# Optimization experiments

Measured on AMD Instinct MI355X. Metric: run time of the kernel, lower is better.

Reference implementation:

```python
import jax, jax.numpy as jnp
import numpy as np

TAU = 0.5

def setup_inputs() -> dict:
    key = jax.random.key(0)
    ks = jax.random.split(key, 20)
    B, D1, D2, E1, E2, U = 4096, 2000, 2000, 256, 256, 512
    M = E1 + E2
    s = lambda k, shp, scale=0.05: jax.random.normal(k, shp, dtype=jnp.float32) * scale
    return {
        "inputs": jax.random.normal(ks[0], (B, D1 + D2), dtype=jnp.float32),
        "h_tm1": jax.random.normal(ks[1], (B, U), dtype=jnp.float32),
        "crohis_tm": jax.random.normal(ks[2], (B, M), dtype=jnp.float32),
        "embed_weight_1": s(ks[3], (D1, E1)),
        "embed_weight_2": s(ks[4], (D2, E2)),
        "ca_1to2_w": s(ks[5], (E1, E1)),
        "ca_1to2_u": s(ks[6], (E2, E1)),
        "ca_1to2_v": s(ks[7], (E2, E1)),
        "ca_2to1_w": s(ks[8], (E2, E2)),
        "ca_2to1_u": s(ks[9], (E1, E2)),
        "ca_2to1_v": s(ks[10], (E1, E2)),
        "crohis_weight_w": s(ks[11], (M, U)),
        "crohis_bias": jnp.zeros((U,), jnp.float32),
        "crohis_decomp_weight": s(ks[12], (M, M)),
        "crohis_decomp_bias": jnp.zeros((M,), jnp.float32),
        "kernel": s(ks[13], (M, 3 * U)),
        "recurrent_kernel": s(ks[14], (U, 3 * U)),
        "bias": jnp.zeros((3 * U,), jnp.float32),
    }


def reference(inputs, h_tm1, crohis_tm,
              embed_weight_1, embed_weight_2,
              ca_1to2_w, ca_1to2_u, ca_1to2_v,
              ca_2to1_w, ca_2to1_u, ca_2to1_v,
              crohis_weight_w, crohis_bias,
              crohis_decomp_weight, crohis_decomp_bias,
              kernel, recurrent_kernel, bias):
    D1 = embed_weight_1.shape[0]
    U = recurrent_kernel.shape[0]
    # dual embedding lookups (dense multi-hot x embedding matrix)
    seqx1 = inputs[:, :D1]
    seqx2 = inputs[:, D1:]
    emb1 = seqx1 @ embed_weight_1   # [B, E1]
    emb2 = seqx2 @ embed_weight_2   # [B, E2]
    # cross-attention gates (softmax over feature axis, as K.softmax default)
    att12 = jax.nn.softmax(jnp.tanh(emb1 @ ca_1to2_w + emb2 @ ca_1to2_u) * (emb2 @ ca_1to2_v), axis=-1)
    att21 = jax.nn.softmax(jnp.tanh(emb2 @ ca_2to1_w + emb1 @ ca_2to1_u) * (emb1 @ ca_2to1_v), axis=-1)
    x = jnp.concatenate([emb1 * att12, emb2 * att21], axis=-1)  # [B, M]
    # cross-history decomposition modulating previous hidden state
    cro = jnp.tanh(crohis_tm @ crohis_decomp_weight + crohis_decomp_bias)
    h_prev = h_tm1 + jnp.tanh(cro @ crohis_weight_w + crohis_bias)
    # GRU (implementation=2, reset_after=False)
    mx = x @ kernel + bias                         # [B, 3U]
    x_z, x_r, x_h = mx[:, :U], mx[:, U:2 * U], mx[:, 2 * U:]
    mi = h_prev @ recurrent_kernel[:, :2 * U]      # [B, 2U]
    z = jax.nn.sigmoid(x_z + mi[:, :U])
    r = jax.nn.sigmoid(x_r + mi[:, U:])
    hh = jnp.tanh(x_h + (r * h_prev) @ recurrent_kernel[:, 2 * U:])
    h = z * h_prev + (1.0 - z) * hh
    # updated cross-history state (exponential moving average with tau)
    crohis_new = TAU * crohis_tm + (1.0 - TAU) * x
    return h, crohis_new
```

## Files before the change

kernel.cpp:

```cpp
#include <hip/hip_runtime.h>
#include <hip/hip_bf16.h>
#include <math.h>


#define TAU_F 0.5f

typedef __bf16 bf16x8 __attribute__((ext_vector_type(8)));
typedef __bf16 bf16x4 __attribute__((ext_vector_type(4)));
typedef float f32x4 __attribute__((ext_vector_type(4)));

__device__ __forceinline__ void gload16(const void* g, void* l) {
    __builtin_amdgcn_global_load_lds(
        (const __attribute__((address_space(1))) void*)g,
        (__attribute__((address_space(3))) void*)l, 16, 0, 0);
}

struct SubGemm {
    const void* A;
    int lda;
    int Kvalid;
    const __bf16* BT;
    int ldbt;
    float* C;
    int ldc;
    long long strideC;
    int Ksub;
    int nbx;
    int pairSplit;
    int pairAOff;
    int obf16;
};

template <bool AFP32>
__global__ __launch_bounds__(256) void gemm_dual(SubGemm g1, SubGemm g2, int blocks1)
{
    __shared__ __attribute__((aligned(16))) char lds[AFP32 ? 16384 : 12288];

    const int tid = threadIdx.x, w = tid >> 6, l = tid & 63;

    const int gx = gridDim.x;
    const int nwg = gx * (int)gridDim.y;
    const int hw = (int)blockIdx.y * gx + (int)blockIdx.x;
    const int lg = (hw & 7) * (nwg >> 3) + (hw >> 3);
    const int bxl_lin = lg % gx;
    const int by = lg / gx;

    const bool second = bxl_lin >= blocks1;
    const SubGemm& g = second ? g2 : g1;
    const int bxl = second ? bxl_lin - blocks1 : bxl_lin;
    const int ct = bxl % g.nbx, spl = bxl / g.nbx;
    const int brow = by * 64, bcol = ct * 128;
    const int k_begin = spl * g.Ksub;
    const int nt = g.Ksub >> 5;
    const int aoff = (ct >= g.pairSplit) ? g.pairAOff : 0;

    const int sbr = w * 32 + (l >> 2);
    const int seg = (l & 3) * 8;

    const __bf16* Bg0 = g.BT + (size_t)(bcol + sbr) * g.ldbt + seg + k_begin;
    const __bf16* Bg1 = Bg0 + (size_t)16 * g.ldbt;

    f32x4 acc[2][4] = {};
    const int fr = l & 15, fk = (l >> 4) * 8;
    const int wr = (w >> 1) * 32, wc = (w & 1) * 64;

    if constexpr (AFP32) {
        auto As32 = (float (*)[32])lds;
        auto Bs   = (__bf16 (*)[32])(lds + 8192);

        const float* Ar0 = (const float*)g.A + aoff
                         + (size_t)(brow + w * 16 + (l >> 3)) * g.lda;
        const float* Ar8 = Ar0 + (size_t)8 * g.lda;
        const int colLane = (l & 7) * 4;
        const int kcl4 = g.Kvalid - 4;

        for (int t = 0; t < nt; ++t) {
            const int k = t * 32;
            __syncthreads();
            int c0 = k_begin + k + colLane;
            c0 = c0 < kcl4 ? c0 : kcl4;
            gload16(Ar0 + c0, &As32[w * 16][0]);
            gload16(Ar8 + c0, &As32[w * 16 + 8][0]);
            gload16(Bg0 + k,  &Bs[w * 32][0]);
            gload16(Bg1 + k,  &Bs[w * 32 + 16][0]);
            __syncthreads();

            bf16x8 a[2], b[4];
#pragma unroll
            for (int m = 0; m < 2; ++m) {
                f32x4 lo = *(const f32x4*)&As32[wr + m * 16 + fr][fk];
                f32x4 hi = *(const f32x4*)&As32[wr + m * 16 + fr][fk + 4];
#pragma unroll
                for (int z = 0; z < 4; ++z) { a[m][z] = (__bf16)lo[z]; a[m][4 + z] = (__bf16)hi[z]; }
            }
#pragma unroll
            for (int n = 0; n < 4; ++n) b[n] = *(const bf16x8*)&Bs[wc + n * 16 + fr][fk];
#pragma unroll
            for (int m = 0; m < 2; ++m)
#pragma unroll
                for (int n = 0; n < 4; ++n)
                    acc[m][n] = __builtin_amdgcn_mfma_f32_16x16x32_bf16(a[m], b[n], acc[m][n], 0, 0, 0);
        }
    } else {
        auto As = (__bf16 (*)[32])lds;
        auto Bs = (__bf16 (*)[32])(lds + 4096);

        const int sar = w * 16 + (l >> 2);
        const __bf16* Ar = (const __bf16*)g.A + aoff
                         + (size_t)(brow + sar) * g.lda + seg + k_begin;

        for (int t = 0; t < nt; ++t) {
            const int k = t * 32;
            __syncthreads();
            gload16(Ar + k,  &As[w * 16][0]);
            gload16(Bg0 + k, &Bs[w * 32][0]);
            gload16(Bg1 + k, &Bs[w * 32 + 16][0]);
            __syncthreads();

            bf16x8 a[2], b[4];
#pragma unroll
            for (int m = 0; m < 2; ++m) a[m] = *(const bf16x8*)&As[wr + m * 16 + fr][fk];
#pragma unroll
            for (int n = 0; n < 4; ++n) b[n] = *(const bf16x8*)&Bs[wc + n * 16 + fr][fk];
#pragma unroll
            for (int m = 0; m < 2; ++m)
#pragma unroll
                for (int n = 0; n < 4; ++n)
                    acc[m][n] = __builtin_amdgcn_mfma_f32_16x16x32_bf16(a[m], b[n], acc[m][n], 0, 0, 0);
        }
    }

    const int fq = (l >> 4) * 4;
    if (g.obf16) {
        __bf16* Cb = (__bf16*)g.C + (size_t)spl * g.strideC;
#pragma unroll
        for (int m = 0; m < 2; ++m)
#pragma unroll
            for (int n = 0; n < 4; ++n)
#pragma unroll
                for (int r = 0; r < 4; ++r) {
                    int row = brow + wr + m * 16 + fq + r;
                    int col = bcol + wc + n * 16 + fr;
                    Cb[(size_t)row * g.ldc + col] = (__bf16)acc[m][n][r];
                }
    } else {
        float* C = g.C + (size_t)spl * g.strideC;
#pragma unroll
        for (int m = 0; m < 2; ++m)
#pragma unroll
            for (int n = 0; n < 4; ++n)
#pragma unroll
                for (int r = 0; r < 4; ++r) {
                    int row = brow + wr + m * 16 + fq + r;
                    int col = bcol + wc + n * 16 + fr;
                    C[(size_t)row * g.ldc + col] = acc[m][n][r];
                }
    }
}

__global__ __launch_bounds__(256) void prep_wT(
    const float* __restrict__ ew1, const float* __restrict__ ew2,
    const float* __restrict__ w12, const float* __restrict__ u12,
    const float* __restrict__ v12, const float* __restrict__ w21,
    const float* __restrict__ u21, const float* __restrict__ v21,
    const float* __restrict__ cd_w, const float* __restrict__ cw_w,
    const float* __restrict__ kern, const float* __restrict__ rkern,
    __bf16* __restrict__ WT, __bf16* __restrict__ WcatT,
    __bf16* __restrict__ cdT, __bf16* __restrict__ cwT,
    __bf16* __restrict__ kernT, __bf16* __restrict__ rkernT)
{
    __shared__ float tile[64][65];
    const int b = blockIdx.x, tid = threadIdx.x;
    const int tr = tid >> 6, tc = tid & 63;

    const float* src = nullptr;
    int ldsrc = 0, srow0 = 0, scol0 = 0, kvalid = 1 << 30;
    __bf16* dst; int ldd, n0, k0;
    bool zero = false;

    if (b < 256) {
        int q = b; n0 = (q >> 5) * 64; k0 = (q & 31) * 64;
        dst = WT; ldd = 2048; kvalid = 2000; ldsrc = 256; srow0 = k0;
        if (n0 < 256) { src = ew1; scol0 = n0; } else { src = ew2; scol0 = n0 - 256; }
    } else if (b < 384) {
        int q = b - 256; n0 = (q >> 3) * 64; k0 = (q & 7) * 64;
        dst = WcatT; ldd = 512; ldsrc = 256; srow0 = k0 & 255; scol0 = n0 & 255;
        int qn = n0 >> 8; bool khi = k0 >= 256;
        if (qn == 0)      src = khi ? u12 : w12;
        else if (qn == 1) src = khi ? w21 : u21;
        else if (qn == 2) { if (khi) src = v12; else zero = true; }
        else              { if (khi) zero = true; else src = v21; }
    } else if (b < 448) {
        int q = b - 384; n0 = (q >> 3) * 64; k0 = (q & 7) * 64;
        src = cd_w; ldsrc = 512; srow0 = k0; scol0 = n0; dst = cdT; ldd = 512;
    } else if (b < 512) {
        int q = b - 448; n0 = (q >> 3) * 64; k0 = (q & 7) * 64;
        src = cw_w; ldsrc = 512; srow0 = k0; scol0 = n0; dst = cwT; ldd = 512;
    } else if (b < 704) {
        int q = b - 512; n0 = (q >> 3) * 64; k0 = (q & 7) * 64;
        src = kern; ldsrc = 1536; srow0 = k0; scol0 = n0; dst = kernT; ldd = 512;
    } else {
        int q = b - 704; n0 = (q >> 3) * 64; k0 = (q & 7) * 64;
        src = rkern; ldsrc = 1536; srow0 = k0; scol0 = n0; dst = rkernT; ldd = 512;
    }

#pragma unroll
    for (int p = 0; p < 16; ++p) {
        int kr = p * 4 + tr;
        float v = 0.f;
        if (!zero && (srow0 + kr) < kvalid)
            v = src[(size_t)(srow0 + kr) * ldsrc + scol0 + tc];
        tile[kr][tc] = v;
    }
    __syncthreads();
#pragma unroll
    for (int p = 0; p < 16; ++p) {
        int nr = p * 4 + tr;
        dst[(size_t)(n0 + nr) * ldd + k0 + tc] = (__bf16)tile[tc][nr];
    }
}

__global__ __launch_bounds__(256) void reduce_A(
    const float* __restrict__ P12, const float* __restrict__ P4,
    const float* __restrict__ cd_b,
    __bf16* __restrict__ E, __bf16* __restrict__ cro)
{
    const int S = 1 << 21;
    int b = blockIdx.x;
    int i = (((b & 2047) * 256) + threadIdx.x) * 4;
    if (b < 2048) {
        f32x4 p0 = *(const f32x4*)(P12 + i);
        f32x4 p1 = *(const f32x4*)(P12 + S + i);
        f32x4 p2 = *(const f32x4*)(P12 + 2 * S + i);
        f32x4 p3 = *(const f32x4*)(P12 + 3 * S + i);
        __bf16 o[4];
#pragma unroll
        for (int j = 0; j < 4; ++j) o[j] = (__bf16)((p0[j] + p1[j]) + (p2[j] + p3[j]));
        *(bf16x4*)&E[i] = *(bf16x4*)o;
    } else {
        f32x4 p0 = *(const f32x4*)(P4 + i);
        f32x4 p1 = *(const f32x4*)(P4 + S + i);
        int c = i & 511;
        __bf16 o[4];
#pragma unroll
        for (int j = 0; j < 4; ++j) o[j] = (__bf16)tanhf(p0[j] + p1[j] + cd_b[c + j]);
        *(bf16x4*)&cro[i] = *(bf16x4*)o;
    }
}

__global__ __launch_bounds__(256) void fuse1(
    const __bf16* __restrict__ T, const __bf16* __restrict__ E,
    const float* __restrict__ crohis,
    const float* __restrict__ P5a, const float* __restrict__ P5b,
    const float* __restrict__ h_tm1, const float* __restrict__ cw_b,
    __bf16* __restrict__ x, float* __restrict__ cro_out,
    float* __restrict__ hprev, __bf16* __restrict__ hprev_bf)
{
    __shared__ float s4[4];
    int b = blockIdx.x;
    int j = threadIdx.x;
    if (b < 4096) {
        const __bf16* t = T + (size_t)b * 1024;
        float s12 = tanhf((float)t[j])       * (float)t[512 + j];
        float s21 = tanhf((float)t[256 + j]) * (float)t[768 + j];
        float v = s12;
#pragma unroll
        for (int o = 32; o >= 1; o >>= 1) v = fmaxf(v, __shfl_xor(v, o, 64));
        __syncthreads(); if ((j & 63) == 0) s4[j >> 6] = v; __syncthreads();
        float m12 = fmaxf(fmaxf(s4[0], s4[1]), fmaxf(s4[2], s4[3]));
        float e12 = expf(s12 - m12);
        v = e12;
#pragma unroll
        for (int o = 32; o >= 1; o >>= 1) v += __shfl_xor(v, o, 64);
        __syncthreads(); if ((j & 63) == 0) s4[j >> 6] = v; __syncthreads();
        float sum12 = s4[0] + s4[1] + s4[2] + s4[3];
        v = s21;
#pragma unroll
        for (int o = 32; o >= 1; o >>= 1) v = fmaxf(v, __shfl_xor(v, o, 64));
        __syncthreads(); if ((j & 63) == 0) s4[j >> 6] = v; __syncthreads();
        float m21 = fmaxf(fmaxf(s4[0], s4[1]), fmaxf(s4[2], s4[3]));
        float e21 = expf(s21 - m21);
        v = e21;
#pragma unroll
        for (int o = 32; o >= 1; o >>= 1) v += __shfl_xor(v, o, 64);
        __syncthreads(); if ((j & 63) == 0) s4[j >> 6] = v; __syncthreads();
        float sum21 = s4[0] + s4[1] + s4[2] + s4[3];

        size_t b0 = (size_t)b * 512 + j, b1 = b0 + 256;
        float x1 = (float)E[b0] * (e12 / sum12);
        float x2 = (float)E[b1] * (e21 / sum21);
        x[b0] = (__bf16)x1;
        x[b1] = (__bf16)x2;
        cro_out[b0] = TAU_F * crohis[b0] + (1.f - TAU_F) * x1;
        cro_out[b1] = TAU_F * crohis[b1] + (1.f - TAU_F) * x2;
    } else {
        int i = ((b - 4096) * 256 + j) * 4;
        f32x4 p0 = *(const f32x4*)(P5a + i);
        f32x4 p1 = *(const f32x4*)(P5b + i);
        f32x4 ht = *(const f32x4*)(h_tm1 + i);
        int c = i & 511;
        f32x4 o; __bf16 ob[4];
#pragma unroll
        for (int q = 0; q < 4; ++q) {
            float hv = ht[q] + tanhf(p0[q] + p1[q] + cw_b[c + q]);
            o[q] = hv; ob[q] = (__bf16)hv;
        }
        *(f32x4*)(hprev + i) = o;
        *(bf16x4*)&hprev_bf[i] = *(bf16x4*)ob;
    }
}

__global__ __launch_bounds__(256) void gates_k(
    const float* __restrict__ mx, const float* __restrict__ mi2,
    const float* __restrict__ hprev, const float* __restrict__ bias,
    __bf16* __restrict__ rh)
{
    int i = (blockIdx.x * 256 + threadIdx.x) * 4;
    int row = i >> 9, c = i & 511;
    f32x4 a  = *(const f32x4*)(mx + (size_t)row * 1536 + 512 + c);
    f32x4 m  = *(const f32x4*)(mi2 + (size_t)row * 1024 + 512 + c);
    f32x4 hp = *(const f32x4*)(hprev + i);
    f32x4 bb = *(const f32x4*)(bias + 512 + c);
    __bf16 o[4];
#pragma unroll
    for (int q = 0; q < 4; ++q) {
        float r = 1.f / (1.f + expf(-(a[q] + bb[q] + m[q])));
        o[q] = (__bf16)(r * hp[q]);
    }
    *(bf16x4*)&rh[i] = *(bf16x4*)o;
}

__global__ __launch_bounds__(256) void final_k(
    const float* __restrict__ mx, const float* __restrict__ mi2,
    const float* __restrict__ P8a, const float* __restrict__ P8b,
    const float* __restrict__ hprev, const float* __restrict__ bias,
    float* __restrict__ h)
{
    int i = (blockIdx.x * 256 + threadIdx.x) * 4;
    int row = i >> 9, c = i & 511;
    f32x4 xz = *(const f32x4*)(mx + (size_t)row * 1536 + c);
    f32x4 xh = *(const f32x4*)(mx + (size_t)row * 1536 + 1024 + c);
    f32x4 mz = *(const f32x4*)(mi2 + (size_t)row * 1024 + c);
    f32x4 p0 = *(const f32x4*)(P8a + i);
    f32x4 p1 = *(const f32x4*)(P8b + i);
    f32x4 hp = *(const f32x4*)(hprev + i);
    f32x4 bz = *(const f32x4*)(bias + c);
    f32x4 bh = *(const f32x4*)(bias + 1024 + c);
    f32x4 o;
#pragma unroll
    for (int q = 0; q < 4; ++q) {
        float z = 1.f / (1.f + expf(-(xz[q] + bz[q] + mz[q])));
        float hh = tanhf(xh[q] + bh[q] + p0[q] + p1[q]);
        o[q] = z * hp[q] + (1.f - z) * hh;
    }
    *(f32x4*)(h + i) = o;
}

extern "C" void kernel_launch(void* const* d_in, const int* in_sizes, int n_in,
                              void* d_out, int out_size, void* d_ws, size_t ws_size,
                              hipStream_t stream)
{
    (void)in_sizes; (void)n_in; (void)out_size; (void)ws_size;

    const float* inputs = (const float*)d_in[0];
    const float* h_tm1  = (const float*)d_in[1];
    const float* crohis = (const float*)d_in[2];
    const float* ew1    = (const float*)d_in[3];
    const float* ew2    = (const float*)d_in[4];
    const float* ca12w  = (const float*)d_in[5];
    const float* ca12u  = (const float*)d_in[6];
    const float* ca12v  = (const float*)d_in[7];
    const float* ca21w  = (const float*)d_in[8];
    const float* ca21u  = (const float*)d_in[9];
    const float* ca21v  = (const float*)d_in[10];
    const float* cw_w   = (const float*)d_in[11];
    const float* cw_b   = (const float*)d_in[12];
    const float* cd_w   = (const float*)d_in[13];
    const float* cd_b   = (const float*)d_in[14];
    const float* kern   = (const float*)d_in[15];
    const float* rkern  = (const float*)d_in[16];
    const float* bias   = (const float*)d_in[17];

    char* ws = (char*)d_ws;
    const size_t MB = 1 << 20;
    float*  P12      = (float*)(ws + 0);
    float*  P5       = (float*)(ws + 0);
    float*  mi2      = (float*)(ws + 0);
    __bf16* x        = (__bf16*)(ws + 16 * MB);
    __bf16* rh       = (__bf16*)(ws + 16 * MB);
    float*  hprev    = (float*)(ws + 20 * MB);
    __bf16* hprev_bf = (__bf16*)(ws + 28 * MB);
    float*  P4       = (float*)(ws + 32 * MB);
    float*  mx       = (float*)(ws + 32 * MB);
    __bf16* E        = (__bf16*)(ws + 48 * MB);
    __bf16* cro_bf   = (__bf16*)(ws + 52 * MB);
    __bf16* T        = (__bf16*)(ws + 56 * MB);
    float*  P8       = (float*)(ws + 56 * MB);
    __bf16* WT       = (__bf16*)(ws + 72 * MB);
    __bf16* WcatT    = (__bf16*)(ws + 74 * MB);
    __bf16* cdT      = (__bf16*)(ws + 75 * MB);
    __bf16* cwT      = (__bf16*)(ws + 75 * MB + 512 * 1024);
    __bf16* kernT    = (__bf16*)(ws + 76 * MB);
    __bf16* rkernT   = (__bf16*)(ws + 77 * MB + 512 * 1024);

    float* h_out   = (float*)d_out;
    float* cro_out = (float*)d_out + 2 * 1048576;

    const int BIG = 1 << 30;
    const long long S2 = 1ll << 21;

    prep_wT<<<896, 256, 0, stream>>>(ew1, ew2, ca12w, ca12u, ca12v, ca21w,
                                     ca21u, ca21v, cd_w, cw_w, kern, rkern,
                                     WT, WcatT, cdT, cwT, kernT, rkernT);

    SubGemm gA1 = { inputs, 4000, 2000, WT,  2048, P12, 512, S2, 512, 4, 2, 2000, 0 };
    SubGemm gA2 = { crohis,  512,  512, cdT,  512, P4,  512, S2, 256, 4, BIG, 0, 0 };
    gemm_dual<true><<<dim3(24, 64), 256, 0, stream>>>(gA1, gA2, 16);

    reduce_A<<<4096, 256, 0, stream>>>(P12, P4, cd_b, E, cro_bf);

    SubGemm gB1 = { E,      512, 512, WcatT, 512, (float*)T, 1024, 0,  512, 8, BIG, 0, 1 };
    SubGemm gB2 = { cro_bf, 512, 512, cwT,   512, P5,        512,  S2, 256, 4, BIG, 0, 0 };
    gemm_dual<false><<<dim3(16, 64), 256, 0, stream>>>(gB1, gB2, 8);

    fuse1<<<6144, 256, 0, stream>>>(T, E, crohis, P5, P5 + S2, h_tm1, cw_b,
                                    x, cro_out, hprev, hprev_bf);

    SubGemm gC1 = { x,        512, 512, kernT,  512, mx,  1536, 0, 512, 12, BIG, 0, 0 };
    SubGemm gC2 = { hprev_bf, 512, 512, rkernT, 512, mi2, 1024, 0, 512, 8,  BIG, 0, 0 };
    gemm_dual<false><<<dim3(20, 64), 256, 0, stream>>>(gC1, gC2, 12);

    gates_k<<<2048, 256, 0, stream>>>(mx, mi2, hprev, bias, rh);

    SubGemm gG = { rh, 512, 512, rkernT + (size_t)1024 * 512, 512, P8, 512, S2, 256, 4, BIG, 0, 0 };
    gemm_dual<false><<<dim3(8, 64), 256, 0, stream>>>(gG, gG, 8);

    final_k<<<2048, 256, 0, stream>>>(mx, mi2, P8, P8 + S2, hprev, bias, h_out);
}
```

Baseline: 143.3 us.

## Load GEMM fragments straight from global to registers and cut split-K factors

```diff
diff --git a/kernel.cpp b/kernel.cpp
--- a/kernel.cpp
+++ b/kernel.cpp
@@ -8,12 +8,6 @@
 typedef __bf16 bf16x8 __attribute__((ext_vector_type(8)));
 typedef __bf16 bf16x4 __attribute__((ext_vector_type(4)));
 typedef float f32x4 __attribute__((ext_vector_type(4)));
-
-__device__ __forceinline__ void gload16(const void* g, void* l) {
-    __builtin_amdgcn_global_load_lds(
-        (const __attribute__((address_space(1))) void*)g,
-        (__attribute__((address_space(3))) void*)l, 16, 0, 0);
-}
 
 struct SubGemm {
     const void* A;
@@ -34,8 +28,6 @@
 template <bool AFP32>
 __global__ __launch_bounds__(256) void gemm_dual(SubGemm g1, SubGemm g2, int blocks1)
 {
-    __shared__ __attribute__((aligned(16))) char lds[AFP32 ? 16384 : 12288];
-
     const int tid = threadIdx.x, w = tid >> 6, l = tid & 63;
 
     const int gx = gridDim.x;
@@ -54,80 +46,69 @@
     const int nt = g.Ksub >> 5;
     const int aoff = (ct >= g.pairSplit) ? g.pairAOff : 0;
 
-    const int sbr = w * 32 + (l >> 2);
-    const int seg = (l & 3) * 8;
-
-    const __bf16* Bg0 = g.BT + (size_t)(bcol + sbr) * g.ldbt + seg + k_begin;
-    const __bf16* Bg1 = Bg0 + (size_t)16 * g.ldbt;
-
-    f32x4 acc[2][4] = {};
     const int fr = l & 15, fk = (l >> 4) * 8;
     const int wr = (w >> 1) * 32, wc = (w & 1) * 64;
 
-    if constexpr (AFP32) {
-        auto As32 = (float (*)[32])lds;
-        auto Bs   = (__bf16 (*)[32])(lds + 8192);
-
-        const float* Ar0 = (const float*)g.A + aoff
-                         + (size_t)(brow + w * 16 + (l >> 3)) * g.lda;
-        const float* Ar8 = Ar0 + (size_t)8 * g.lda;
-        const int colLane = (l & 7) * 4;
-        const int kcl4 = g.Kvalid - 4;
-
-        for (int t = 0; t < nt; ++t) {
-            const int k = t * 32;
-            __syncthreads();
-            int c0 = k_begin + k + colLane;
-            c0 = c0 < kcl4 ? c0 : kcl4;
-            gload16(Ar0 + c0, &As32[w * 16][0]);
-            gload16(Ar8 + c0, &As32[w * 16 + 8][0]);
-            gload16(Bg0 + k,  &Bs[w * 32][0]);
-            gload16(Bg1 + k,  &Bs[w * 32 + 16][0]);
-            __syncthreads();
-
-            bf16x8 a[2], b[4];
-#pragma unroll
-            for (int m = 0; m < 2; ++m) {
-                f32x4 lo = *(const f32x4*)&As32[wr + m * 16 + fr][fk];
-                f32x4 hi = *(const f32x4*)&As32[wr + m * 16 + fr][fk + 4];
-#pragma unroll
-                for (int z = 0; z < 4; ++z) { a[m][z] = (__bf16)lo[z]; a[m][4 + z] = (__bf16)hi[z]; }
-            }
-#pragma unroll
-            for (int n = 0; n < 4; ++n) b[n] = *(const bf16x8*)&Bs[wc + n * 16 + fr][fk];
-#pragma unroll
-            for (int m = 0; m < 2; ++m)
-#pragma unroll
-                for (int n = 0; n < 4; ++n)
-                    acc[m][n] = __builtin_amdgcn_mfma_f32_16x16x32_bf16(a[m], b[n], acc[m][n], 0, 0, 0);
+    const __bf16* b0 = g.BT + (size_t)(bcol + wc +  0 + fr) * g.ldbt + k_begin + fk;
+    const __bf16* b1 = g.BT + (size_t)(bcol + wc + 16 + fr) * g.ldbt + k_begin + fk;
+    const __bf16* b2 = g.BT + (size_t)(bcol + wc + 32 + fr) * g.ldbt + k_begin + fk;
+    const __bf16* b3 = g.BT + (size_t)(bcol + wc + 48 + fr) * g.ldbt + k_begin + fk;
+
+    const __bf16* a0b = (const __bf16*)g.A + aoff + (size_t)(brow + wr +  0 + fr) * g.lda + k_begin + fk;
+    const __bf16* a1b = (const __bf16*)g.A + aoff + (size_t)(brow + wr + 16 + fr) * g.lda + k_begin + fk;
+    const float*  a0f = (const float*)g.A + aoff + (size_t)(brow + wr +  0 + fr) * g.lda;
+    const float*  a1f = (const float*)g.A + aoff + (size_t)(brow + wr + 16 + fr) * g.lda;
+    const int kcl = g.Kvalid - 8;
+
+    struct FR { bf16x8 a0, a1, b0, b1, b2, b3; };
+
+    auto ldA32 = [&](const float* rowp, int k) -> bf16x8 {
+        int c = k_begin + k + fk;
+        c = c < kcl ? c : kcl;
+        f32x4 lo = *(const f32x4*)(rowp + c);
+        f32x4 hi = *(const f32x4*)(rowp + c + 4);
+        bf16x8 r;
+#pragma unroll
+        for (int z = 0; z < 4; ++z) { r[z] = (__bf16)lo[z]; r[4 + z] = (__bf16)hi[z]; }
+        return r;
+    };
+
+    auto LD = [&](int k) -> FR {
+        FR f;
+        if constexpr (AFP32) {
+            f.a0 = ldA32(a0f, k);
+            f.a1 = ldA32(a1f, k);
+        } else {
+            f.a0 = *(const bf16x8*)(a0b + k);
+            f.a1 = *(const bf16x8*)(a1b + k);
         }
-    } else {
-        auto As = (__bf16 (*)[32])lds;
-        auto Bs = (__bf16 (*)[32])(lds + 4096);
-
-        const int sar = w * 16 + (l >> 2);
-        const __bf16* Ar = (const __bf16*)g.A + aoff
-                         + (size_t)(brow + sar) * g.lda + seg + k_begin;
-
-        for (int t = 0; t < nt; ++t) {
-            const int k = t * 32;
-            __syncthreads();
-            gload16(Ar + k,  &As[w * 16][0]);
-            gload16(Bg0 + k, &Bs[w * 32][0]);
-            gload16(Bg1 + k, &Bs[w * 32 + 16][0]);
-            __syncthreads();
-
-            bf16x8 a[2], b[4];
-#pragma unroll
-            for (int m = 0; m < 2; ++m) a[m] = *(const bf16x8*)&As[wr + m * 16 + fr][fk];
-#pragma unroll
-            for (int n = 0; n < 4; ++n) b[n] = *(const bf16x8*)&Bs[wc + n * 16 + fr][fk];
-#pragma unroll
-            for (int m = 0; m < 2; ++m)
-#pragma unroll
-                for (int n = 0; n < 4; ++n)
-                    acc[m][n] = __builtin_amdgcn_mfma_f32_16x16x32_bf16(a[m], b[n], acc[m][n], 0, 0, 0);
-        }
+        f.b0 = *(const bf16x8*)(b0 + k);
+        f.b1 = *(const bf16x8*)(b1 + k);
+        f.b2 = *(const bf16x8*)(b2 + k);
+        f.b3 = *(const bf16x8*)(b3 + k);
+        return f;
+    };
+
+    f32x4 acc[2][4] = {};
+    auto MM = [&](const FR& f) {
+        acc[0][0] = __builtin_amdgcn_mfma_f32_16x16x32_bf16(f.a0, f.b0, acc[0][0], 0, 0, 0);
+        acc[0][1] = __builtin_amdgcn_mfma_f32_16x16x32_bf16(f.a0, f.b1, acc[0][1], 0, 0, 0);
+        acc[0][2] = __builtin_amdgcn_mfma_f32_16x16x32_bf16(f.a0, f.b2, acc[0][2], 0, 0, 0);
+        acc[0][3] = __builtin_amdgcn_mfma_f32_16x16x32_bf16(f.a0, f.b3, acc[0][3], 0, 0, 0);
+        acc[1][0] = __builtin_amdgcn_mfma_f32_16x16x32_bf16(f.a1, f.b0, acc[1][0], 0, 0, 0);
+        acc[1][1] = __builtin_amdgcn_mfma_f32_16x16x32_bf16(f.a1, f.b1, acc[1][1], 0, 0, 0);
+        acc[1][2] = __builtin_amdgcn_mfma_f32_16x16x32_bf16(f.a1, f.b2, acc[1][2], 0, 0, 0);
+        acc[1][3] = __builtin_amdgcn_mfma_f32_16x16x32_bf16(f.a1, f.b3, acc[1][3], 0, 0, 0);
+    };
+
+    FR f0 = LD(0);
+    const int klast = (nt - 1) * 32;
+    for (int t = 0; t < nt; t += 2) {
+        FR f1 = LD((t + 1) * 32);
+        MM(f0);
+        int k2 = (t + 2) * 32;
+        f0 = LD(k2 < klast ? k2 : klast);
+        MM(f1);
     }
 
     const int fq = (l >> 4) * 4;
@@ -231,19 +212,16 @@
     if (b < 2048) {
         f32x4 p0 = *(const f32x4*)(P12 + i);
         f32x4 p1 = *(const f32x4*)(P12 + S + i);
-        f32x4 p2 = *(const f32x4*)(P12 + 2 * S + i);
-        f32x4 p3 = *(const f32x4*)(P12 + 3 * S + i);
         __bf16 o[4];
 #pragma unroll
-        for (int j = 0; j < 4; ++j) o[j] = (__bf16)((p0[j] + p1[j]) + (p2[j] + p3[j]));
+        for (int j = 0; j < 4; ++j) o[j] = (__bf16)(p0[j] + p1[j]);
         *(bf16x4*)&E[i] = *(bf16x4*)o;
     } else {
         f32x4 p0 = *(const f32x4*)(P4 + i);
-        f32x4 p1 = *(const f32x4*)(P4 + S + i);
         int c = i & 511;
         __bf16 o[4];
 #pragma unroll
-        for (int j = 0; j < 4; ++j) o[j] = (__bf16)tanhf(p0[j] + p1[j] + cd_b[c + j]);
+        for (int j = 0; j < 4; ++j) o[j] = (__bf16)tanhf(p0[j] + cd_b[c + j]);
         *(bf16x4*)&cro[i] = *(bf16x4*)o;
     }
 }
@@ -251,7 +229,7 @@
 __global__ __launch_bounds__(256) void fuse1(
     const __bf16* __restrict__ T, const __bf16* __restrict__ E,
     const float* __restrict__ crohis,
-    const float* __restrict__ P5a, const float* __restrict__ P5b,
+    const float* __restrict__ P5,
     const float* __restrict__ h_tm1, const float* __restrict__ cw_b,
     __bf16* __restrict__ x, float* __restrict__ cro_out,
     float* __restrict__ hprev, __bf16* __restrict__ hprev_bf)
@@ -295,14 +273,13 @@
         cro_out[b1] = TAU_F * crohis[b1] + (1.f - TAU_F) * x2;
     } else {
         int i = ((b - 4096) * 256 + j) * 4;
-        f32x4 p0 = *(const f32x4*)(P5a + i);
-        f32x4 p1 = *(const f32x4*)(P5b + i);
+        f32x4 p = *(const f32x4*)(P5 + i);
         f32x4 ht = *(const f32x4*)(h_tm1 + i);
         int c = i & 511;
         f32x4 o; __bf16 ob[4];
 #pragma unroll
         for (int q = 0; q < 4; ++q) {
-            float hv = ht[q] + tanhf(p0[q] + p1[q] + cw_b[c + q]);
+            float hv = ht[q] + tanhf(p[q] + cw_b[c + q]);
             o[q] = hv; ob[q] = (__bf16)hv;
         }
         *(f32x4*)(hprev + i) = o;
@@ -413,17 +390,17 @@
                                      ca21u, ca21v, cd_w, cw_w, kern, rkern,
                                      WT, WcatT, cdT, cwT, kernT, rkernT);
 
-    SubGemm gA1 = { inputs, 4000, 2000, WT,  2048, P12, 512, S2, 512, 4, 2, 2000, 0 };
-    SubGemm gA2 = { crohis,  512,  512, cdT,  512, P4,  512, S2, 256, 4, BIG, 0, 0 };
-    gemm_dual<true><<<dim3(24, 64), 256, 0, stream>>>(gA1, gA2, 16);
+    SubGemm gA1 = { inputs, 4000, 2000, WT,  2048, P12, 512, S2, 1024, 4, 2, 2000, 0 };
+    SubGemm gA2 = { crohis,  512,  512, cdT,  512, P4,  512, 0,   512, 4, BIG, 0, 0 };
+    gemm_dual<true><<<dim3(12, 64), 256, 0, stream>>>(gA1, gA2, 8);
 
     reduce_A<<<4096, 256, 0, stream>>>(P12, P4, cd_b, E, cro_bf);
 
-    SubGemm gB1 = { E,      512, 512, WcatT, 512, (float*)T, 1024, 0,  512, 8, BIG, 0, 1 };
-    SubGemm gB2 = { cro_bf, 512, 512, cwT,   512, P5,        512,  S2, 256, 4, BIG, 0, 0 };
-    gemm_dual<false><<<dim3(16, 64), 256, 0, stream>>>(gB1, gB2, 8);
-
-    fuse1<<<6144, 256, 0, stream>>>(T, E, crohis, P5, P5 + S2, h_tm1, cw_b,
+    SubGemm gB1 = { E,      512, 512, WcatT, 512, (float*)T, 1024, 0, 512, 8, BIG, 0, 1 };
+    SubGemm gB2 = { cro_bf, 512, 512, cwT,   512, P5,        512,  0, 512, 4, BIG, 0, 0 };
+    gemm_dual<false><<<dim3(12, 64), 256, 0, stream>>>(gB1, gB2, 8);
+
+    fuse1<<<6144, 256, 0, stream>>>(T, E, crohis, P5, h_tm1, cw_b,
                                     x, cro_out, hprev, hprev_bf);
 
     SubGemm gC1 = { x,        512, 512, kernT,  512, mx,  1536, 0, 512, 12, BIG, 0, 0 };
```

Result: slower. 234.5 us (+63.6%).
